# Performance work log

Measured on AMD Instinct MI355X. Metric: run time of the kernel, lower is better.

Reference implementation:

```python
import jax, jax.numpy as jnp
import numpy as np


def setup_inputs() -> dict:
    key = jax.random.key(0)
    k1, k2 = jax.random.split(key)
    B, P = 32, 1024
    pred = jax.random.normal(k1, (B, 2 * P), dtype=jnp.float32)
    truth = jax.random.normal(k2, (B, 2 * P), dtype=jnp.float32)
    return {"pred": pred, "truth": truth}


def reference(pred, truth):
    # pred, truth: [B, 2P]; first P cols = X coords, last P = Y coords.
    B = pred.shape[0]
    P = pred.shape[1] // 2
    # diffPred - diffTruth for anchor ix equals d - d[:, ix:ix+1] where d = pred - truth,
    # so the whole loop fuses into one broadcasted pairwise difference.
    d = pred - truth                      # [B, 2P]
    dX, dY = d[:, :P], d[:, P:]

    def per_anchor_dists(v):
        # diff[b, i, j] = v[b, j] - v[b, i]  (i = anchor ix)
        diff = v[:, None, :] - v[:, :, None]          # [B, P, P]
        return jnp.sqrt(jnp.sum(diff * diff, axis=(0, 2)))  # [P] Frobenius dist per ix

    total = jnp.sum(per_anchor_dists(dX)) + jnp.sum(per_anchor_dists(dY))
    return total / (B * 2.0)
```

## Files before the change

### kernel.cpp

```cpp
#include <hip/hip_runtime.h>
#include <math.h>

#define BB 32
#define PP 1024
#define WW 2048


__device__ __forceinline__ float wave_reduce_sum(float v) {
    #pragma unroll
    for (int off = 32; off > 0; off >>= 1)
        v += __shfl_down(v, off, 64);
    return v;
}

__global__ void k1_row_stats(const float* __restrict__ pred,
                             const float* __restrict__ truth,
                             float* __restrict__ ws) {
    const int bid = blockIdx.x;
    const int h = bid >> 5;
    const int b = bid & 31;
    const int base = b * WW + h * PP;
    const int t = threadIdx.x;

    float s = 0.f, q = 0.f;
    #pragma unroll
    for (int k = 0; k < 4; ++k) {
        const int j = t + k * 256;
        const float x = pred[base + j] - truth[base + j];
        s += x;
        q += x * x;
    }
    s = wave_reduce_sum(s);
    q = wave_reduce_sum(q);

    __shared__ float ls[4], lq[4];
    const int wave = t >> 6, lane = t & 63;
    if (lane == 0) { ls[wave] = s; lq[wave] = q; }
    __syncthreads();
    if (t == 0) {
        ws[bid]      = ls[0] + ls[1] + ls[2] + ls[3];
        ws[64 + bid] = lq[0] + lq[1] + lq[2] + lq[3];
    }
}

__global__ void k2_anchor(const float* __restrict__ pred,
                          const float* __restrict__ truth,
                          float* __restrict__ ws) {
    const int h = blockIdx.x;
    const int i = threadIdx.x;

    float T = 0.f;
    #pragma unroll
    for (int k = 0; k < BB; ++k) T += ws[64 + h * 32 + k];

    __shared__ float Ssh[BB];
    if (i < BB) Ssh[i] = ws[h * 32 + i];
    __syncthreads();

    float q = 0.f, r = 0.f;
    #pragma unroll
    for (int b = 0; b < BB; ++b) {
        const int idx = b * WW + h * PP + i;
        const float x = pred[idx] - truth[idx];
        q += x * x;
        r += x * Ssh[b];
    }
    const float D = T + (float)PP * q - 2.f * r;
    float s = sqrtf(fmaxf(D, 0.f));

    s = wave_reduce_sum(s);
    __shared__ float lp[16];
    const int wave = i >> 6, lane = i & 63;
    if (lane == 0) lp[wave] = s;
    __syncthreads();
    if (i == 0) {
        float tot = 0.f;
        #pragma unroll
        for (int w = 0; w < 16; ++w) tot += lp[w];
        ws[128 + h] = tot;
    }
}

__global__ void k3_finish(const float* __restrict__ ws, float* __restrict__ out) {
    if (threadIdx.x == 0)
        out[0] = (ws[128] + ws[129]) * (1.0f / 64.0f);
}

extern "C" void kernel_launch(void* const* d_in, const int* in_sizes, int n_in,
                              void* d_out, int out_size, void* d_ws, size_t ws_size,
                              hipStream_t stream) {
    const float* pred  = (const float*)d_in[0];
    const float* truth = (const float*)d_in[1];
    float* ws  = (float*)d_ws;
    float* out = (float*)d_out;

    k1_row_stats<<<64, 256, 0, stream>>>(pred, truth, ws);
    k2_anchor<<<2, 1024, 0, stream>>>(pred, truth, ws);
    k3_finish<<<1, 64, 0, stream>>>(ws, out);
}
```

Before: 59.88 us.

## Fuse three kernels into one single-block kernel with float4 row sums

Replaces the three-kernel pipeline (row stats, anchor distances, finish) with one 1024-thread block that loops over both coordinate halves. It computes row sums with float4 loads, then the per-anchor sums and the block reductions, and writes the final result directly. This removes two kernel launches and the workspace round-trips. In exchange all work runs on one CU instead of up to 64 blocks, so memory bandwidth parallelism drops and the two halves run serially.

Result: slower. 64.23 us (+7.3%).

```diff
diff --git a/kernel.cpp b/kernel.cpp
--- a/kernel.cpp
+++ b/kernel.cpp
@@ -4,7 +4,6 @@
 #define BB 32
 #define PP 1024
 #define WW 2048
-
 
 __device__ __forceinline__ float wave_reduce_sum(float v) {
     #pragma unroll
@@ -13,77 +12,70 @@
     return v;
 }
 
-__global__ void k1_row_stats(const float* __restrict__ pred,
-                             const float* __restrict__ truth,
-                             float* __restrict__ ws) {
-    const int bid = blockIdx.x;
-    const int h = bid >> 5;
-    const int b = bid & 31;
-    const int base = b * WW + h * PP;
+__global__ void __launch_bounds__(1024)
+gcs_fused(const float* __restrict__ pred,
+          const float* __restrict__ truth,
+          float* __restrict__ out) {
     const int t = threadIdx.x;
-
-    float s = 0.f, q = 0.f;
-    #pragma unroll
-    for (int k = 0; k < 4; ++k) {
-        const int j = t + k * 256;
-        const float x = pred[base + j] - truth[base + j];
-        s += x;
-        q += x * x;
-    }
-    s = wave_reduce_sum(s);
-    q = wave_reduce_sum(q);
-
-    __shared__ float ls[4], lq[4];
-    const int wave = t >> 6, lane = t & 63;
-    if (lane == 0) { ls[wave] = s; lq[wave] = q; }
-    __syncthreads();
-    if (t == 0) {
-        ws[bid]      = ls[0] + ls[1] + ls[2] + ls[3];
-        ws[64 + bid] = lq[0] + lq[1] + lq[2] + lq[3];
-    }
-}
-
-__global__ void k2_anchor(const float* __restrict__ pred,
-                          const float* __restrict__ truth,
-                          float* __restrict__ ws) {
-    const int h = blockIdx.x;
-    const int i = threadIdx.x;
-
-    float T = 0.f;
-    #pragma unroll
-    for (int k = 0; k < BB; ++k) T += ws[64 + h * 32 + k];
+    const int wave = t >> 6;
+    const int lane = t & 63;
 
     __shared__ float Ssh[BB];
-    if (i < BB) Ssh[i] = ws[h * 32 + i];
-    __syncthreads();
+    __shared__ float red[16];
 
-    float q = 0.f, r = 0.f;
-    #pragma unroll
-    for (int b = 0; b < BB; ++b) {
-        const int idx = b * WW + h * PP + i;
-        const float x = pred[idx] - truth[idx];
-        q += x * x;
-        r += x * Ssh[b];
+    float grand = 0.f;
+
+    for (int h = 0; h < 2; ++h) {
+        const int hbase = h * PP;
+
+        #pragma unroll
+        for (int rr = 0; rr < 2; ++rr) {
+            const int b = wave * 2 + rr;
+            const float4* p4 = (const float4*)(pred + b * WW + hbase);
+            const float4* t4 = (const float4*)(truth + b * WW + hbase);
+            float s = 0.f;
+            #pragma unroll
+            for (int k = 0; k < 4; ++k) {
+                const int j = lane + 64 * k;
+                const float4 a = p4[j], c = t4[j];
+                s += (a.x - c.x) + (a.y - c.y) + (a.z - c.z) + (a.w - c.w);
+            }
+            s = wave_reduce_sum(s);
+            if (lane == 0) Ssh[b] = s;
+        }
+        __syncthreads();
+
+        float q = 0.f, r = 0.f;
+        #pragma unroll
+        for (int b = 0; b < BB; ++b) {
+            const int idx = b * WW + hbase + t;
+            const float x = pred[idx] - truth[idx];
+            q = fmaf(x, x, q);
+            r = fmaf(x, Ssh[b], r);
+        }
+
+        float qs = wave_reduce_sum(q);
+        if (lane == 0) red[wave] = qs;
+        __syncthreads();
+        float T = 0.f;
+        #pragma unroll
+        for (int w = 0; w < 16; ++w) T += red[w];
+
+        const float si = sqrtf(fmaxf(T + (float)PP * q - 2.f * r, 0.f));
+        float ss = wave_reduce_sum(si);
+        __syncthreads();
+        if (lane == 0) red[wave] = ss;
+        __syncthreads();
+        if (t == 0) {
+            float tot = 0.f;
+            #pragma unroll
+            for (int w = 0; w < 16; ++w) tot += red[w];
+            grand += tot;
+        }
+        __syncthreads();
     }
-    const float D = T + (float)PP * q - 2.f * r;
-    float s = sqrtf(fmaxf(D, 0.f));
 
-    s = wave_reduce_sum(s);
-    __shared__ float lp[16];
-    const int wave = i >> 6, lane = i & 63;
-    if (lane == 0) lp[wave] = s;
-    __syncthreads();
-    if (i == 0) {
-        float tot = 0.f;
-        #pragma unroll
-        for (int w = 0; w < 16; ++w) tot += lp[w];
-        ws[128 + h] = tot;
-    }
-}
-
-__global__ void k3_finish(const float* __restrict__ ws, float* __restrict__ out) {
-    if (threadIdx.x == 0)
-        out[0] = (ws[128] + ws[129]) * (1.0f / 64.0f);
+    if (t == 0) out[0] = grand * (1.0f / 64.0f);
 }
 
 extern "C" void kernel_launch(void* const* d_in, const int* in_sizes, int n_in,
@@ -91,10 +83,7 @@
                               hipStream_t stream) {
     const float* pred  = (const float*)d_in[0];
     const float* truth = (const float*)d_in[1];
-    float* ws  = (float*)d_ws;
     float* out = (float*)d_out;
 
-    k1_row_stats<<<64, 256, 0, stream>>>(pred, truth, ws);
-    k2_anchor<<<2, 1024, 0, stream>>>(pred, truth, ws);
-    k3_finish<<<1, 64, 0, stream>>>(ws, out);
+    gcs_fused<<<1, 1024, 0, stream>>>(pred, truth, out);
 }
```
